# Kernel tuning notes

Hardware: AMD Instinct MI355X
Metric: run time of the kernel (lower is better)

## Reference

```python
import jax, jax.numpy as jnp
import numpy as np

EMBED_DIM = 1024
BATCH, SEQ = 4, 2048


def setup_inputs() -> dict:
    key = jax.random.key(0)
    k1, k2 = jax.random.split(key)
    hidden_states = jax.random.normal(k1, (BATCH, SEQ, EMBED_DIM), dtype=jnp.float32)
    # fused QKV projection weight (Linear(embed_dim, 3*embed_dim, bias=False)),
    # stored as [E, 3E] so y = x @ W
    W_qkv = jax.random.normal(k2, (EMBED_DIM, 3 * EMBED_DIM), dtype=jnp.float32) * (1.0 / np.sqrt(EMBED_DIM))
    return {"hidden_states": hidden_states, "W_qkv": W_qkv}


def reference(hidden_states, W_qkv):
    E = hidden_states.shape[-1]
    scale = 1.0 / np.sqrt(E)
    qkv = jnp.einsum('bse,ef->bsf', hidden_states, W_qkv)  # [B,S,3E]
    q, k, v = jnp.split(qkv, 3, axis=-1)                   # each [B,S,E]
    # scores = q @ (k^T * scale); softmax over keys
    scores = jnp.einsum('bqe,bke->bqk', q, k) * scale      # [B,S,S]
    w = jax.nn.softmax(scores, axis=-1)
    return jnp.einsum('bqk,bke->bqe', w, v)                # [B,S,E]
```

## Files before the change

### kernel.cpp

```cpp
#include <hip/hip_runtime.h>

typedef __attribute__((ext_vector_type(8))) short short8;
typedef __attribute__((ext_vector_type(8))) unsigned short ushort8;
typedef __attribute__((ext_vector_type(4))) float f32x4;

__device__ __forceinline__ float bf2f(unsigned short u) {
  union { unsigned int u; float f; } c; c.u = ((unsigned int)u) << 16; return c.f;
}
__device__ __forceinline__ unsigned short f2bf(float f) {
  union { float f; unsigned int u; } c; c.f = f;
  unsigned int x = c.u;
  return (unsigned short)((x + 0x7FFFu + ((x >> 16) & 1u)) >> 16);
}

#define GLD_LDS16(g, l)                                                        \
  __builtin_amdgcn_global_load_lds(                                            \
      (const __attribute__((address_space(1))) void*)(g),                      \
      (__attribute__((address_space(3))) void*)(l), 16, 0, 0)

__device__ __forceinline__ void bar() {
  asm volatile("" ::: "memory");
  __builtin_amdgcn_s_barrier();
  asm volatile("" ::: "memory");
}

__global__ __launch_bounds__(256) void prep_kernel(
    const float* __restrict__ X, unsigned short* __restrict__ Xb,
    const float* __restrict__ W, unsigned short* __restrict__ Wt,
    float* __restrict__ Lrow) {
  const int t = threadIdx.x;
  if (blockIdx.x < 4096) {
    long i = ((long)blockIdx.x * 256 + t) * 8;
    float4 a = *(const float4*)(X + i);
    float4 b = *(const float4*)(X + i + 4);
    ushort8 o;
    o[0] = f2bf(a.x); o[1] = f2bf(a.y); o[2] = f2bf(a.z); o[3] = f2bf(a.w);
    o[4] = f2bf(b.x); o[5] = f2bf(b.y); o[6] = f2bf(b.z); o[7] = f2bf(b.w);
    *(ushort8*)(Xb + i) = o;
  } else if (blockIdx.x < 4864) {
    const int bid = blockIdx.x - 4096;
    const int f0 = (bid % 48) * 64;
    const int e0 = (bid / 48) * 64;
    __shared__ unsigned short tile[64][65];
    const int cg = (t & 15) * 4;
    const int r = t >> 4;
#pragma unroll
    for (int i = 0; i < 4; ++i) {
      int e = r + i * 16;
      float4 v = *(const float4*)(W + (long)(e0 + e) * 3072 + f0 + cg);
      tile[e][cg + 0] = f2bf(v.x);
      tile[e][cg + 1] = f2bf(v.y);
      tile[e][cg + 2] = f2bf(v.z);
      tile[e][cg + 3] = f2bf(v.w);
    }
    __syncthreads();
#pragma unroll
    for (int i = 0; i < 4; ++i) {
      int f = (t >> 4) + i * 16;
      int e = (t & 15) * 4;
      ushort4 o;
      o.x = tile[e + 0][f];
      o.y = tile[e + 1][f];
      o.z = tile[e + 2][f];
      o.w = tile[e + 3][f];
      *(ushort4*)(Wt + (long)(f0 + f) * 1024 + e0 + e) = o;
    }
  } else {
    float4 z = {0.f, 0.f, 0.f, 0.f};
#pragma unroll
    for (int j = 0; j < 8; ++j) *(float4*)(Lrow + (j * 256 + t) * 4) = z;
  }
}

template <int MODE>
__device__ __forceinline__ void gemm256_body(
    const unsigned short* __restrict__ A, const unsigned short* __restrict__ B,
    void* __restrict__ Cv, int K, int lda, int ldb, int ldc,
    long sA, long sB, long sC, float alpha, float* __restrict__ Lrow,
    unsigned short* __restrict__ Vt) {
  __shared__ __align__(16) unsigned short smem[65536];

  const int t = threadIdx.x;
  const int lane = t & 63;
  const int wave = t >> 6;
  const int quad = lane >> 4;
  const int mrow = lane & 15;
  const int wm = wave >> 2;
  const int wn = wave & 3;

  const int bx = blockIdx.x, by = blockIdx.y, b = blockIdx.z;
  const int rowA0 = by * 256;
  const int rowB0 = bx * 256;
  const unsigned short* Ab = A + (long)b * sA;
  const unsigned short* Bb = B + (long)b * sB;

  const int srow = lane >> 3;
  const int scol = ((lane & 7) ^ srow) * 8;

  const unsigned short* gA[4];
  const unsigned short* gB[4];
#pragma unroll
  for (int j = 0; j < 4; ++j) {
    gA[j] = Ab + (long)(rowA0 + j * 64 + wave * 8 + srow) * lda + scol;
    gB[j] = Bb + (long)(rowB0 + j * 64 + wave * 8 + srow) * ldb + scol;
  }
  const int dst = wave * 512;

  f32x4 acc[8][4];
#pragma unroll
  for (int i = 0; i < 8; ++i)
#pragma unroll
    for (int j = 0; j < 4; ++j) {
      f32x4 z = {0.f, 0.f, 0.f, 0.f};
      acc[i][j] = z;
    }

  const int NT = K >> 6;

  const int m7 = mrow & 7;
  const int aslot0 = (quad ^ m7) * 8;
  const int arow0 = (wm * 128 + mrow) * 64;
  const int brow0 = (wn * 64 + mrow) * 64;

  short8 aC[4], aN[4], bC[4], bN[4];

  {
#pragma unroll
    for (int j = 0; j < 4; ++j) GLD_LDS16(gA[j], smem + j * 4096 + dst);
#pragma unroll
    for (int j = 0; j < 4; ++j)
      GLD_LDS16(gB[j], smem + 16384 + j * 4096 + dst);
    asm volatile("s_waitcnt vmcnt(0)" ::: "memory");
    bar();
#pragma unroll
    for (int i = 0; i < 4; ++i)
      aC[i] = *(const short8*)(smem + arow0 + i * 1024 + aslot0);
#pragma unroll
    for (int j = 0; j < 4; ++j)
      bC[j] = *(const short8*)(smem + 16384 + brow0 + j * 1024 + aslot0);
  }

  for (int T = 0; T < NT; ++T) {
    const int boff = (T & 1) << 15;
    const int noff = boff ^ 32768;
    const unsigned short* As = smem + boff;
    const unsigned short* Bs = smem + boff + 16384;
    const unsigned short* Asn = smem + noff;
    const unsigned short* Bsn = smem + noff + 16384;
    const int kt1 = (T + 1) << 6;
    const bool more = (T + 1) < NT;

#pragma unroll
    for (int i = 0; i < 4; ++i)
      aN[i] = *(const short8*)(As + arow0 + 4096 + i * 1024 + aslot0);
    if (more) {
      GLD_LDS16(gA[0] + kt1, smem + noff + 0 * 4096 + dst);
      GLD_LDS16(gA[2] + kt1, smem + noff + 2 * 4096 + dst);
      GLD_LDS16(gB[0] + kt1, smem + noff + 16384 + 0 * 4096 + dst);
      GLD_LDS16(gB[1] + kt1, smem + noff + 16384 + 1 * 4096 + dst);
      GLD_LDS16(gB[2] + kt1, smem + noff + 16384 + 2 * 4096 + dst);
      GLD_LDS16(gB[3] + kt1, smem + noff + 16384 + 3 * 4096 + dst);
    }
    bar();
    asm volatile("s_waitcnt lgkmcnt(4)" ::: "memory");
    __builtin_amdgcn_sched_barrier(0);
    __builtin_amdgcn_s_setprio(1);
#pragma unroll
    for (int i = 0; i < 4; ++i)
#pragma unroll
      for (int j = 0; j < 4; ++j)
        acc[i][j] = __builtin_amdgcn_mfma_f32_16x16x32_bf16(aC[i], bC[j],
                                                            acc[i][j], 0, 0, 0);
    __builtin_amdgcn_s_setprio(0);

#pragma unroll
    for (int i = 0; i < 4; ++i)
      aC[i] = *(const short8*)(As + arow0 + i * 1024 + (aslot0 ^ 32));
#pragma unroll
    for (int j = 0; j < 4; ++j)
      bN[j] = *(const short8*)(Bs + brow0 + j * 1024 + (aslot0 ^ 32));
    if (more) {
      GLD_LDS16(gA[1] + kt1, smem + noff + 1 * 4096 + dst);
      GLD_LDS16(gA[3] + kt1, smem + noff + 3 * 4096 + dst);
    }
    bar();
    asm volatile("s_waitcnt lgkmcnt(8)" ::: "memory");
    __builtin_amdgcn_sched_barrier(0);
    __builtin_amdgcn_s_setprio(1);
#pragma unroll
    for (int i = 0; i < 4; ++i)
#pragma unroll
      for (int j = 0; j < 4; ++j)
        acc[4 + i][j] = __builtin_amdgcn_mfma_f32_16x16x32_bf16(
            aN[i], bC[j], acc[4 + i][j], 0, 0, 0);
    __builtin_amdgcn_s_setprio(0);

#pragma unroll
    for (int i = 0; i < 4; ++i)
      aN[i] = *(const short8*)(As + arow0 + 4096 + i * 1024 + (aslot0 ^ 32));
    if (more) asm volatile("s_waitcnt vmcnt(2)" ::: "memory");
    bar();
    asm volatile("s_waitcnt lgkmcnt(4)" ::: "memory");
    __builtin_amdgcn_sched_barrier(0);
    __builtin_amdgcn_s_setprio(1);
#pragma unroll
    for (int i = 0; i < 4; ++i)
#pragma unroll
      for (int j = 0; j < 4; ++j)
        acc[i][j] = __builtin_amdgcn_mfma_f32_16x16x32_bf16(aC[i], bN[j],
                                                            acc[i][j], 0, 0, 0);
    __builtin_amdgcn_s_setprio(0);

    if (more) {
#pragma unroll
      for (int i = 0; i < 4; ++i)
        aC[i] = *(const short8*)(Asn + arow0 + i * 1024 + aslot0);
#pragma unroll
      for (int j = 0; j < 4; ++j)
        bC[j] = *(const short8*)(Bsn + brow0 + j * 1024 + aslot0);
      asm volatile("s_waitcnt vmcnt(0)" ::: "memory");
    }
    bar();
    if (more) {
      asm volatile("s_waitcnt lgkmcnt(8)" ::: "memory");
    } else {
      asm volatile("s_waitcnt lgkmcnt(0)" ::: "memory");
    }
    __builtin_amdgcn_sched_barrier(0);
    __builtin_amdgcn_s_setprio(1);
#pragma unroll
    for (int i = 0; i < 4; ++i)
#pragma unroll
      for (int j = 0; j < 4; ++j)
        acc[4 + i][j] = __builtin_amdgcn_mfma_f32_16x16x32_bf16(
            aN[i], bN[j], acc[4 + i][j], 0, 0, 0);
    __builtin_amdgcn_s_setprio(0);
  }

  const long cb = (long)b * sC;

  if constexpr (MODE == 0) {
    if (bx < 8) {
      unsigned short* C = (unsigned short*)Cv;
#pragma unroll
      for (int m = 0; m < 8; ++m) {
        int row = rowA0 + wm * 128 + m * 16 + quad * 4;
#pragma unroll
        for (int j = 0; j < 4; ++j) {
          int col = rowB0 + wn * 64 + j * 16 + mrow;
#pragma unroll
          for (int r = 0; r < 4; ++r)
            C[(long)(row + r) * ldc + col] = f2bf(acc[m][j][r]);
        }
      }
    } else {
      bar();
#pragma unroll
      for (int m = 0; m < 8; ++m) {
        int s4 = wm * 128 + m * 16 + quad * 4;
#pragma unroll
        for (int j = 0; j < 4; ++j) {
          int e = wn * 64 + j * 16 + mrow;
          int swz = ((e & 7) << 4) ^ (((e >> 3) & 3) << 3);
          ushort4 pk;
          pk.x = f2bf(acc[m][j][0]);
          pk.y = f2bf(acc[m][j][1]);
          pk.z = f2bf(acc[m][j][2]);
          pk.w = f2bf(acc[m][j][3]);
          *(ushort4*)(smem + e * 256 + (s4 ^ swz)) = pk;
        }
      }
      __syncthreads();
      const int batch = by >> 3;
      const int s_base = (by & 7) * 256;
      const int e_base = (bx - 8) * 256;
      unsigned short* VtB = Vt + (long)batch * 1024 * 2048;
      const int er = t >> 5;
      const int s = (t & 31) * 8;
#pragma unroll
      for (int rnd = 0; rnd < 16; ++rnd) {
        int e = rnd * 16 + er;
        int swz = ((e & 7) << 4) ^ (((e >> 3) & 3) << 3);
        ushort8 v = *(const ushort8*)(smem + e * 256 + (s ^ swz));
        *(ushort8*)(VtB + (long)(e_base + e) * 2048 + s_base + s) = v;
      }
    }
  } else {
    unsigned short* C = (unsigned short*)Cv;
    float p[8][4];
#pragma unroll
    for (int m = 0; m < 8; ++m)
#pragma unroll
      for (int r = 0; r < 4; ++r) p[m][r] = 0.f;
#pragma unroll
    for (int m = 0; m < 8; ++m) {
      int row = rowA0 + wm * 128 + m * 16 + quad * 4;
#pragma unroll
      for (int j = 0; j < 4; ++j) {
        int col = rowB0 + wn * 64 + j * 16 + mrow;
#pragma unroll
        for (int r = 0; r < 4; ++r) {
          float e = __expf(acc[m][j][r] * alpha);
          C[cb + (long)(row + r) * ldc + col] = f2bf(e);
          p[m][r] += e;
        }
      }
    }
#pragma unroll
    for (int off = 1; off < 16; off <<= 1)
#pragma unroll
      for (int m = 0; m < 8; ++m)
#pragma unroll
        for (int r = 0; r < 4; ++r)
          p[m][r] += __shfl_xor(p[m][r], off, 64);
    if (mrow == 0) {
#pragma unroll
      for (int m = 0; m < 8; ++m) {
        int row = rowA0 + wm * 128 + m * 16 + quad * 4;
#pragma unroll
        for (int r = 0; r < 4; ++r)
          atomicAdd(&Lrow[b * 2048 + row + r], p[m][r]);
      }
    }
  }
}

template <int MODE>
__device__ __forceinline__ void gemm_body(
    const unsigned short* __restrict__ A, const unsigned short* __restrict__ B,
    void* __restrict__ Cv, int K, int lda, int ldb, int ldc,
    long sA, long sB, long sC, float alpha, float* __restrict__ Lrow,
    unsigned short* __restrict__ Vt) {
  constexpr int BM = 128, BN = 128, BK = 64;
  __shared__ __align__(16) unsigned short smem[BM * BK + BN * BK];
  unsigned short* As = smem;
  unsigned short* Bs = smem + BM * BK;

  const int t = threadIdx.x;
  const int lane = t & 63;
  const int wave = t >> 6;
  const int quad = lane >> 4;
  const int mrow = lane & 15;
  const int wm = wave >> 1, wn = wave & 1;

  const int bx = blockIdx.x, by = blockIdx.y;
  const int rowA0 = by * BM;
  const int rowB0 = bx * BN;
  const int b = blockIdx.z;
  const unsigned short* Ab = A + (long)b * sA;
  const unsigned short* Bb = B + (long)b * sB;

  f32x4 acc[4][4];
#pragma unroll
  for (int i = 0; i < 4; ++i)
#pragma unroll
    for (int j = 0; j < 4; ++j) {
      f32x4 z = {0.f, 0.f, 0.f, 0.f};
      acc[i][j] = z;
    }

  const int rbase = wave * 32 + (lane >> 3);
  const int c2 = lane & 7;

  for (int kt = 0; kt < K; kt += BK) {
#pragma unroll
    for (int j = 0; j < 4; ++j) {
      int r = rbase + j * 8;
      int c = c2 ^ (r & 7);
      GLD_LDS16(Ab + (long)(rowA0 + r) * lda + kt + c * 8, As + (wave * 4 + j) * 512);
      GLD_LDS16(Bb + (long)(rowB0 + r) * ldb + kt + c * 8, Bs + (wave * 4 + j) * 512);
    }
    __syncthreads();
#pragma unroll
    for (int ks = 0; ks < 2; ++ks) {
      short8 af[4], bfr[4];
#pragma unroll
      for (int i = 0; i < 4; ++i) {
        int rA = wm * 64 + i * 16 + mrow;
        int cc = ks * 4 + quad;
        af[i] = *(const short8*)(As + (rA * 8 + (cc ^ (rA & 7))) * 8);
        int rB = wn * 64 + i * 16 + mrow;
        bfr[i] = *(const short8*)(Bs + (rB * 8 + (cc ^ (rB & 7))) * 8);
      }
#pragma unroll
      for (int mt = 0; mt < 4; ++mt)
#pragma unroll
        for (int nt = 0; nt < 4; ++nt)
          acc[mt][nt] = __builtin_amdgcn_mfma_f32_16x16x32_bf16(
              af[mt], bfr[nt], acc[mt][nt], 0, 0, 0);
    }
    __syncthreads();
  }

  const int m_base = rowA0 + wm * 64;
  const int n_base = rowB0 + wn * 64;
  const long cb = (long)b * sC;

#pragma unroll
  for (int mt = 0; mt < 4; ++mt)
#pragma unroll
    for (int i = 0; i < 4; ++i) {
      int row = m_base + mt * 16 + quad * 4 + i;
      float inv = 1.0f / Lrow[b * 2048 + row];
#pragma unroll
      for (int nt = 0; nt < 4; ++nt) {
        int col = n_base + nt * 16 + mrow;
        ((float*)Cv)[cb + (long)row * ldc + col] = acc[mt][nt][i] * inv;
      }
    }
}

__global__ __launch_bounds__(512, 2) void qkv_gemm_kernel(
    const unsigned short* __restrict__ A, const unsigned short* __restrict__ B,
    void* __restrict__ Cv, int K, int lda, int ldb, int ldc,
    long sA, long sB, long sC, float alpha, float* __restrict__ Lrow,
    unsigned short* __restrict__ Vt) {
  gemm256_body<0>(A, B, Cv, K, lda, ldb, ldc, sA, sB, sC, alpha, Lrow, Vt);
}
__global__ __launch_bounds__(512, 2) void score_gemm_kernel(
    const unsigned short* __restrict__ A, const unsigned short* __restrict__ B,
    void* __restrict__ Cv, int K, int lda, int ldb, int ldc,
    long sA, long sB, long sC, float alpha, float* __restrict__ Lrow,
    unsigned short* __restrict__ Vt) {
  gemm256_body<1>(A, B, Cv, K, lda, ldb, ldc, sA, sB, sC, alpha, Lrow, Vt);
}
__global__ __launch_bounds__(256, 2) void out_gemm_kernel(
    const unsigned short* __restrict__ A, const unsigned short* __restrict__ B,
    void* __restrict__ Cv, int K, int lda, int ldb, int ldc,
    long sA, long sB, long sC, float alpha, float* __restrict__ Lrow,
    unsigned short* __restrict__ Vt) {
  gemm_body<2>(A, B, Cv, K, lda, ldb, ldc, sA, sB, sC, alpha, Lrow, Vt);
}

extern "C" void kernel_launch(void* const* d_in, const int* in_sizes, int n_in,
                              void* d_out, int out_size, void* d_ws, size_t ws_size,
                              hipStream_t stream) {
  const float* X = (const float*)d_in[0];
  const float* W = (const float*)d_in[1];
  float* out = (float*)d_out;

  char* ws = (char*)d_ws;
  unsigned short* Xb  = (unsigned short*)(ws);
  unsigned short* Wtb = (unsigned short*)(ws + 16777216);
  unsigned short* QK  = (unsigned short*)(ws + 23068672);
  unsigned short* Vt  = (unsigned short*)(ws + 56623104);
  unsigned short* Sb  = (unsigned short*)(ws + 73400320);
  float* Lrow         = (float*)(ws + 106954752);

  prep_kernel<<<4865, 256, 0, stream>>>(X, Xb, W, Wtb, Lrow);

  qkv_gemm_kernel<<<dim3(12, 32, 1), 512, 0, stream>>>(
      Xb, Wtb, QK, 1024, 1024, 1024, 2048, 0L, 0L, 0L, 1.0f, nullptr, Vt);

  score_gemm_kernel<<<dim3(8, 8, 4), 512, 0, stream>>>(
      QK, QK + 1024, Sb, 1024, 2048, 2048, 2048,
      (long)2048 * 2048, (long)2048 * 2048, (long)2048 * 2048, 0.03125f, Lrow, nullptr);

  out_gemm_kernel<<<dim3(8, 16, 4), 256, 0, stream>>>(
      Sb, Vt, out, 2048, 2048, 2048, 1024,
      (long)2048 * 2048, (long)1024 * 2048, (long)2048 * 1024, 1.0f, Lrow, nullptr);
}
```

Before: 239.1 us.

## Replace 256x256 four-phase GEMM with simpler 256x128 double-buffered GEMM

The QKV and score GEMMs switch from a 256x256 tile with a hand-interleaved four-phase LDS/MFMA pipeline to a 256x128 tile with a plain double-buffered loop. That loop loads all fragments for the step, runs 32 MFMAs, then waits and synchronizes with a single barrier. Grids double in x and the V-transpose epilogue is adapted to the narrower tile. The aim is more blocks for better CU occupancy and load balance with less register pressure. The cost is lower per-block data reuse and giving up the finer overlap and priority hints of the previous pipeline.

```diff
diff --git a/kernel.cpp b/kernel.cpp
--- a/kernel.cpp
+++ b/kernel.cpp
@@ -73,24 +73,24 @@
 }
 
 template <int MODE>
-__device__ __forceinline__ void gemm256_body(
-    const unsigned short* __restrict__ A, const unsigned short* __restrict__ B,
-    void* __restrict__ Cv, int K, int lda, int ldb, int ldc,
-    long sA, long sB, long sC, float alpha, float* __restrict__ Lrow,
-    unsigned short* __restrict__ Vt) {
-  __shared__ __align__(16) unsigned short smem[65536];
+__device__ __forceinline__ void gemm2ph_body(
+    const unsigned short* __restrict__ A, const unsigned short* __restrict__ B,
+    void* __restrict__ Cv, int K, int lda, int ldb, int ldc,
+    long sA, long sB, long sC, float alpha, float* __restrict__ Lrow,
+    unsigned short* __restrict__ Vt) {
+  __shared__ __align__(16) unsigned short smem[49152];
 
   const int t = threadIdx.x;
   const int lane = t & 63;
   const int wave = t >> 6;
   const int quad = lane >> 4;
   const int mrow = lane & 15;
-  const int wm = wave >> 2;
-  const int wn = wave & 3;
+  const int wm = wave >> 1;
+  const int wn = wave & 1;
 
   const int bx = blockIdx.x, by = blockIdx.y, b = blockIdx.z;
   const int rowA0 = by * 256;
-  const int rowB0 = bx * 256;
+  const int rowB0 = bx * 128;
   const unsigned short* Ab = A + (long)b * sA;
   const unsigned short* Bb = B + (long)b * sB;
 
@@ -98,17 +98,19 @@
   const int scol = ((lane & 7) ^ srow) * 8;
 
   const unsigned short* gA[4];
-  const unsigned short* gB[4];
-#pragma unroll
-  for (int j = 0; j < 4; ++j) {
-    gA[j] = Ab + (long)(rowA0 + j * 64 + wave * 8 + srow) * lda + scol;
-    gB[j] = Bb + (long)(rowB0 + j * 64 + wave * 8 + srow) * ldb + scol;
-  }
-  const int dst = wave * 512;
-
-  f32x4 acc[8][4];
-#pragma unroll
-  for (int i = 0; i < 8; ++i)
+  const unsigned short* gB[2];
+#pragma unroll
+  for (int g = 0; g < 4; ++g)
+    gA[g] = Ab + (long)(rowA0 + wave * 32 + g * 8 + srow) * lda + scol;
+#pragma unroll
+  for (int g = 0; g < 2; ++g)
+    gB[g] = Bb + (long)(rowB0 + wave * 16 + g * 8 + srow) * ldb + scol;
+  const int dstA = wave * 2048;
+  const int dstB = 16384 + wave * 1024;
+
+  f32x4 acc[4][4];
+#pragma unroll
+  for (int i = 0; i < 4; ++i)
 #pragma unroll
     for (int j = 0; j < 4; ++j) {
       f32x4 z = {0.f, 0.f, 0.f, 0.f};
@@ -117,168 +119,97 @@
 
   const int NT = K >> 6;
 
-  const int m7 = mrow & 7;
-  const int aslot0 = (quad ^ m7) * 8;
-  const int arow0 = (wm * 128 + mrow) * 64;
-  const int brow0 = (wn * 64 + mrow) * 64;
-
-  short8 aC[4], aN[4], bC[4], bN[4];
-
-  {
-#pragma unroll
-    for (int j = 0; j < 4; ++j) GLD_LDS16(gA[j], smem + j * 4096 + dst);
-#pragma unroll
-    for (int j = 0; j < 4; ++j)
-      GLD_LDS16(gB[j], smem + 16384 + j * 4096 + dst);
+#pragma unroll
+  for (int g = 0; g < 4; ++g) GLD_LDS16(gA[g], smem + dstA + g * 512);
+#pragma unroll
+  for (int g = 0; g < 2; ++g) GLD_LDS16(gB[g], smem + dstB + g * 512);
+  asm volatile("s_waitcnt vmcnt(0)" ::: "memory");
+  bar();
+
+  const int aslot0 = (quad ^ (mrow & 7)) * 8;
+  int cur = 0, nxt = 24576;
+
+  for (int T = 0; T < NT; ++T) {
+    const int kt1 = (T + 1) << 6;
+    if (T + 1 < NT) {
+#pragma unroll
+      for (int g = 0; g < 4; ++g)
+        GLD_LDS16(gA[g] + kt1, smem + nxt + dstA + g * 512);
+#pragma unroll
+      for (int g = 0; g < 2; ++g)
+        GLD_LDS16(gB[g] + kt1, smem + nxt + dstB + g * 512);
+    }
+    short8 a0[4], a1[4], b0[4], b1[4];
+#pragma unroll
+    for (int i = 0; i < 4; ++i) {
+      const int ra = cur + (wm * 64 + i * 16 + mrow) * 64;
+      a0[i] = *(const short8*)(smem + ra + aslot0);
+      a1[i] = *(const short8*)(smem + ra + (aslot0 ^ 32));
+    }
+#pragma unroll
+    for (int j = 0; j < 4; ++j) {
+      const int rb = cur + 16384 + (wn * 64 + j * 16 + mrow) * 64;
+      b0[j] = *(const short8*)(smem + rb + aslot0);
+      b1[j] = *(const short8*)(smem + rb + (aslot0 ^ 32));
+    }
+#pragma unroll
+    for (int i = 0; i < 4; ++i)
+#pragma unroll
+      for (int j = 0; j < 4; ++j)
+        acc[i][j] = __builtin_amdgcn_mfma_f32_16x16x32_bf16(a0[i], b0[j],
+                                                            acc[i][j], 0, 0, 0);
+#pragma unroll
+    for (int i = 0; i < 4; ++i)
+#pragma unroll
+      for (int j = 0; j < 4; ++j)
+        acc[i][j] = __builtin_amdgcn_mfma_f32_16x16x32_bf16(a1[i], b1[j],
+                                                            acc[i][j], 0, 0, 0);
     asm volatile("s_waitcnt vmcnt(0)" ::: "memory");
     bar();
-#pragma unroll
-    for (int i = 0; i < 4; ++i)
-      aC[i] = *(const short8*)(smem + arow0 + i * 1024 + aslot0);
-#pragma unroll
-    for (int j = 0; j < 4; ++j)
-      bC[j] = *(const short8*)(smem + 16384 + brow0 + j * 1024 + aslot0);
+    int tmp = cur; cur = nxt; nxt = tmp;
   }
 
-  for (int T = 0; T < NT; ++T) {
-    const int boff = (T & 1) << 15;
-    const int noff = boff ^ 32768;
-    const unsigned short* As = smem + boff;
-    const unsigned short* Bs = smem + boff + 16384;
-    const unsigned short* Asn = smem + noff;
-    const unsigned short* Bsn = smem + noff + 16384;
-    const int kt1 = (T + 1) << 6;
-    const bool more = (T + 1) < NT;
-
-#pragma unroll
-    for (int i = 0; i < 4; ++i)
-      aN[i] = *(const short8*)(As + arow0 + 4096 + i * 1024 + aslot0);
-    if (more) {
-      GLD_LDS16(gA[0] + kt1, smem + noff + 0 * 4096 + dst);
-      GLD_LDS16(gA[2] + kt1, smem + noff + 2 * 4096 + dst);
-      GLD_LDS16(gB[0] + kt1, smem + noff + 16384 + 0 * 4096 + dst);
-      GLD_LDS16(gB[1] + kt1, smem + noff + 16384 + 1 * 4096 + dst);
-      GLD_LDS16(gB[2] + kt1, smem + noff + 16384 + 2 * 4096 + dst);
-      GLD_LDS16(gB[3] + kt1, smem + noff + 16384 + 3 * 4096 + dst);
-    }
-    bar();
-    asm volatile("s_waitcnt lgkmcnt(4)" ::: "memory");
-    __builtin_amdgcn_sched_barrier(0);
-    __builtin_amdgcn_s_setprio(1);
-#pragma unroll
-    for (int i = 0; i < 4; ++i)
-#pragma unroll
-      for (int j = 0; j < 4; ++j)
-        acc[i][j] = __builtin_amdgcn_mfma_f32_16x16x32_bf16(aC[i], bC[j],
-                                                            acc[i][j], 0, 0, 0);
-    __builtin_amdgcn_s_setprio(0);
-
-#pragma unroll
-    for (int i = 0; i < 4; ++i)
-      aC[i] = *(const short8*)(As + arow0 + i * 1024 + (aslot0 ^ 32));
-#pragma unroll
-    for (int j = 0; j < 4; ++j)
-      bN[j] = *(const short8*)(Bs + brow0 + j * 1024 + (aslot0 ^ 32));
-    if (more) {
-      GLD_LDS16(gA[1] + kt1, smem + noff + 1 * 4096 + dst);
-      GLD_LDS16(gA[3] + kt1, smem + noff + 3 * 4096 + dst);
-    }
-    bar();
-    asm volatile("s_waitcnt lgkmcnt(8)" ::: "memory");
-    __builtin_amdgcn_sched_barrier(0);
-    __builtin_amdgcn_s_setprio(1);
-#pragma unroll
-    for (int i = 0; i < 4; ++i)
-#pragma unroll
-      for (int j = 0; j < 4; ++j)
-        acc[4 + i][j] = __builtin_amdgcn_mfma_f32_16x16x32_bf16(
-            aN[i], bC[j], acc[4 + i][j], 0, 0, 0);
-    __builtin_amdgcn_s_setprio(0);
-
-#pragma unroll
-    for (int i = 0; i < 4; ++i)
-      aN[i] = *(const short8*)(As + arow0 + 4096 + i * 1024 + (aslot0 ^ 32));
-    if (more) asm volatile("s_waitcnt vmcnt(2)" ::: "memory");
-    bar();
-    asm volatile("s_waitcnt lgkmcnt(4)" ::: "memory");
-    __builtin_amdgcn_sched_barrier(0);
-    __builtin_amdgcn_s_setprio(1);
-#pragma unroll
-    for (int i = 0; i < 4; ++i)
-#pragma unroll
-      for (int j = 0; j < 4; ++j)
-        acc[i][j] = __builtin_amdgcn_mfma_f32_16x16x32_bf16(aC[i], bN[j],
-                                                            acc[i][j], 0, 0, 0);
-    __builtin_amdgcn_s_setprio(0);
-
-    if (more) {
-#pragma unroll
-      for (int i = 0; i < 4; ++i)
-        aC[i] = *(const short8*)(Asn + arow0 + i * 1024 + aslot0);
-#pragma unroll
-      for (int j = 0; j < 4; ++j)
-        bC[j] = *(const short8*)(Bsn + brow0 + j * 1024 + aslot0);
-      asm volatile("s_waitcnt vmcnt(0)" ::: "memory");
-    }
-    bar();
-    if (more) {
-      asm volatile("s_waitcnt lgkmcnt(8)" ::: "memory");
-    } else {
-      asm volatile("s_waitcnt lgkmcnt(0)" ::: "memory");
-    }
-    __builtin_amdgcn_sched_barrier(0);
-    __builtin_amdgcn_s_setprio(1);
-#pragma unroll
-    for (int i = 0; i < 4; ++i)
-#pragma unroll
-      for (int j = 0; j < 4; ++j)
-        acc[4 + i][j] = __builtin_amdgcn_mfma_f32_16x16x32_bf16(
-            aN[i], bN[j], acc[4 + i][j], 0, 0, 0);
-    __builtin_amdgcn_s_setprio(0);
-  }
-
   const long cb = (long)b * sC;
 
   if constexpr (MODE == 0) {
-    if (bx < 8) {
+    if (bx < 16) {
       unsigned short* C = (unsigned short*)Cv;
 #pragma unroll
-      for (int m = 0; m < 8; ++m) {
-        int row = rowA0 + wm * 128 + m * 16 + quad * 4;
+      for (int i = 0; i < 4; ++i) {
+        int row = rowA0 + wm * 64 + i * 16 + quad * 4;
 #pragma unroll
         for (int j = 0; j < 4; ++j) {
           int col = rowB0 + wn * 64 + j * 16 + mrow;
 #pragma unroll
           for (int r = 0; r < 4; ++r)
-            C[(long)(row + r) * ldc + col] = f2bf(acc[m][j][r]);
+            C[(long)(row + r) * ldc + col] = f2bf(acc[i][j][r]);
         }
       }
     } else {
-      bar();
-#pragma unroll
-      for (int m = 0; m < 8; ++m) {
-        int s4 = wm * 128 + m * 16 + quad * 4;
+#pragma unroll
+      for (int i = 0; i < 4; ++i) {
+        int s4 = wm * 64 + i * 16 + quad * 4;
 #pragma unroll
         for (int j = 0; j < 4; ++j) {
           int e = wn * 64 + j * 16 + mrow;
           int swz = ((e & 7) << 4) ^ (((e >> 3) & 3) << 3);
           ushort4 pk;
-          pk.x = f2bf(acc[m][j][0]);
-          pk.y = f2bf(acc[m][j][1]);
-          pk.z = f2bf(acc[m][j][2]);
-          pk.w = f2bf(acc[m][j][3]);
+          pk.x = f2bf(acc[i][j][0]);
+          pk.y = f2bf(acc[i][j][1]);
+          pk.z = f2bf(acc[i][j][2]);
+          pk.w = f2bf(acc[i][j][3]);
           *(ushort4*)(smem + e * 256 + (s4 ^ swz)) = pk;
         }
       }
       __syncthreads();
       const int batch = by >> 3;
       const int s_base = (by & 7) * 256;
-      const int e_base = (bx - 8) * 256;
+      const int e_base = (bx - 16) * 128;
       unsigned short* VtB = Vt + (long)batch * 1024 * 2048;
       const int er = t >> 5;
       const int s = (t & 31) * 8;
 #pragma unroll
-      for (int rnd = 0; rnd < 16; ++rnd) {
+      for (int rnd = 0; rnd < 8; ++rnd) {
         int e = rnd * 16 + er;
         int swz = ((e & 7) << 4) ^ (((e >> 3) & 3) << 3);
         ushort8 v = *(const ushort8*)(smem + e * 256 + (s ^ swz));
@@ -287,39 +218,39 @@
     }
   } else {
     unsigned short* C = (unsigned short*)Cv;
-    float p[8][4];
-#pragma unroll
-    for (int m = 0; m < 8; ++m)
-#pragma unroll
-      for (int r = 0; r < 4; ++r) p[m][r] = 0.f;
-#pragma unroll
-    for (int m = 0; m < 8; ++m) {
-      int row = rowA0 + wm * 128 + m * 16 + quad * 4;
+    float p[4][4];
+#pragma unroll
+    for (int i = 0; i < 4; ++i)
+#pragma unroll
+      for (int r = 0; r < 4; ++r) p[i][r] = 0.f;
+#pragma unroll
+    for (int i = 0; i < 4; ++i) {
+      int row = rowA0 + wm * 64 + i * 16 + quad * 4;
 #pragma unroll
       for (int j = 0; j < 4; ++j) {
         int col = rowB0 + wn * 64 + j * 16 + mrow;
 #pragma unroll
         for (int r = 0; r < 4; ++r) {
-          float e = __expf(acc[m][j][r] * alpha);
+          float e = __expf(acc[i][j][r] * alpha);
           C[cb + (long)(row + r) * ldc + col] = f2bf(e);
-          p[m][r] += e;
+          p[i][r] += e;
         }
       }
     }
 #pragma unroll
     for (int off = 1; off < 16; off <<= 1)
 #pragma unroll
-      for (int m = 0; m < 8; ++m)
+      for (int i = 0; i < 4; ++i)
 #pragma unroll
         for (int r = 0; r < 4; ++r)
-          p[m][r] += __shfl_xor(p[m][r], off, 64);
+          p[i][r] += __shfl_xor(p[i][r], off, 64);
     if (mrow == 0) {
 #pragma unroll
-      for (int m = 0; m < 8; ++m) {
-        int row = rowA0 + wm * 128 + m * 16 + quad * 4;
+      for (int i = 0; i < 4; ++i) {
+        int row = rowA0 + wm * 64 + i * 16 + quad * 4;
 #pragma unroll
         for (int r = 0; r < 4; ++r)
-          atomicAdd(&Lrow[b * 2048 + row + r], p[m][r]);
+          atomicAdd(&Lrow[b * 2048 + row + r], p[i][r]);
       }
     }
   }
@@ -415,14 +346,14 @@
     void* __restrict__ Cv, int K, int lda, int ldb, int ldc,
     long sA, long sB, long sC, float alpha, float* __restrict__ Lrow,
     unsigned short* __restrict__ Vt) {
-  gemm256_body<0>(A, B, Cv, K, lda, ldb, ldc, sA, sB, sC, alpha, Lrow, Vt);
+  gemm2ph_body<0>(A, B, Cv, K, lda, ldb, ldc, sA, sB, sC, alpha, Lrow, Vt);
 }
 __global__ __launch_bounds__(512, 2) void score_gemm_kernel(
     const unsigned short* __restrict__ A, const unsigned short* __restrict__ B,
     void* __restrict__ Cv, int K, int lda, int ldb, int ldc,
     long sA, long sB, long sC, float alpha, float* __restrict__ Lrow,
     unsigned short* __restrict__ Vt) {
-  gemm256_body<1>(A, B, Cv, K, lda, ldb, ldc, sA, sB, sC, alpha, Lrow, Vt);
+  gemm2ph_body<1>(A, B, Cv, K, lda, ldb, ldc, sA, sB, sC, alpha, Lrow, Vt);
 }
 __global__ __launch_bounds__(256, 2) void out_gemm_kernel(
     const unsigned short* __restrict__ A, const unsigned short* __restrict__ B,
@@ -449,10 +380,10 @@
 
   prep_kernel<<<4865, 256, 0, stream>>>(X, Xb, W, Wtb, Lrow);
 
-  qkv_gemm_kernel<<<dim3(12, 32, 1), 512, 0, stream>>>(
+  qkv_gemm_kernel<<<dim3(24, 32, 1), 512, 0, stream>>>(
       Xb, Wtb, QK, 1024, 1024, 1024, 2048, 0L, 0L, 0L, 1.0f, nullptr, Vt);
 
-  score_gemm_kernel<<<dim3(8, 8, 4), 512, 0, stream>>>(
+  score_gemm_kernel<<<dim3(16, 8, 4), 512, 0, stream>>>(
       QK, QK + 1024, Sb, 1024, 2048, 2048, 2048,
       (long)2048 * 2048, (long)2048 * 2048, (long)2048 * 2048, 0.03125f, Lrow, nullptr);
 
```

New measurement: 242.2 us. No clear change (+1.3%).
